# Optimization experiments

Hardware: AMD Instinct MI355X
Metric: run time of the kernel (lower is better)

## Reference

```python
import jax, jax.numpy as jnp
import numpy as np
from jax import lax

N, IN_CH, H, W = 8, 128, 160, 160
NUM_ANCHORS = 9
ANCHOR_SIZES = (32.0, 64.0, 128.0)
ANCHOR_RATIOS = (0.5, 1.0, 2.0)
NMS_THRESH = 0.7
PRE_NMS_TOPK = 6000
POST_NMS_TOPK = 1000
MIN_SIZE = 0.0
SCALE_CLAMP = float(np.log(1000.0 / 16.0))  # detectron2 Box2BoxTransform clamp


def setup_inputs():
    key = jax.random.key(0)
    k = jax.random.split(key, 4)
    std = 0.01  # nn.init.normal_(l.weight, std=0.01), bias = 0
    return {
        "feature_map": jax.random.normal(k[0], (N, IN_CH, H, W), jnp.float32),
        "conv1_w": jax.random.normal(k[1], (IN_CH, IN_CH, 3, 3), jnp.float32) * std,
        "conv1_b": jnp.zeros((IN_CH,), jnp.float32),
        "cls_w": jax.random.normal(k[2], (NUM_ANCHORS, IN_CH, 1, 1), jnp.float32) * std,
        "cls_b": jnp.zeros((NUM_ANCHORS,), jnp.float32),
        "box_w": jax.random.normal(k[3], (NUM_ANCHORS * 4, IN_CH, 1, 1), jnp.float32) * std,
        "box_b": jnp.zeros((NUM_ANCHORS * 4,), jnp.float32),
        "image_size": 1280,
    }


def _conv(x, w, b, pad):
    y = lax.conv_general_dilated(x, w, (1, 1), pad, dimension_numbers=("NCHW", "OIHW", "NCHW"))
    return y + b[None, :, None, None]


def _make_anchors(stride):
    # base anchors: area = size^2, w = sqrt(area/ratio), h = w*ratio (detectron2 style)
    base = []
    for s in ANCHOR_SIZES:
        area = s * s
        for r in ANCHOR_RATIOS:
            bw = np.sqrt(area / r)
            bh = bw * r
            base.append([-bw / 2.0, -bh / 2.0, bw / 2.0, bh / 2.0])
    base = jnp.asarray(np.array(base, np.float32))  # [A,4]
    sx = jnp.arange(W, dtype=jnp.float32) * stride
    sy = jnp.arange(H, dtype=jnp.float32) * stride
    yy, xx = jnp.meshgrid(sy, sx, indexing="ij")
    shifts = jnp.stack([xx, yy, xx, yy], axis=-1).reshape(-1, 1, 4)  # [H*W,1,4]
    return (shifts + base[None]).reshape(-1, 4)  # [H*W*A,4], (H,W,A) order


def _decode(deltas, anchors):
    # Box2BoxTransform.apply_deltas with weights (1,1,1,1)
    wa = anchors[:, 2] - anchors[:, 0]
    ha = anchors[:, 3] - anchors[:, 1]
    cxa = anchors[:, 0] + 0.5 * wa
    cya = anchors[:, 1] + 0.5 * ha
    dx, dy = deltas[..., 0], deltas[..., 1]
    dw = jnp.minimum(deltas[..., 2], SCALE_CLAMP)
    dh = jnp.minimum(deltas[..., 3], SCALE_CLAMP)
    cx = dx * wa + cxa
    cy = dy * ha + cya
    w = jnp.exp(dw) * wa
    h = jnp.exp(dh) * ha
    return jnp.stack([cx - 0.5 * w, cy - 0.5 * h, cx + 0.5 * w, cy + 0.5 * h], axis=-1)


def _nms_per_image(boxes, scores, image_size):
    # boxes [M,4], scores [M] -> top-PRE_NMS_TOPK, clip, filter, greedy NMS, keep POST_NMS_TOPK
    k = min(PRE_NMS_TOPK, scores.shape[0])
    top_scores, idx = lax.top_k(scores, k)
    b = jnp.clip(boxes[idx], 0.0, image_size)
    bw = b[:, 2] - b[:, 0]
    bh = b[:, 3] - b[:, 1]
    valid = (bw >= MIN_SIZE) & (bh >= MIN_SIZE)
    sc0 = jnp.where(valid, top_scores, -jnp.inf)
    areas = bw * bh

    def body(sc, _):
        i = jnp.argmax(sc)
        s = sc[i]
        bi = b[i]
        ix1 = jnp.maximum(bi[0], b[:, 0])
        iy1 = jnp.maximum(bi[1], b[:, 1])
        ix2 = jnp.minimum(bi[2], b[:, 2])
        iy2 = jnp.minimum(bi[3], b[:, 3])
        inter = jnp.maximum(ix2 - ix1, 0.0) * jnp.maximum(iy2 - iy1, 0.0)
        iou = inter / jnp.maximum(areas[i] + areas - inter, 1e-9)
        sc = jnp.where(iou > NMS_THRESH, -jnp.inf, sc)  # also suppresses self
        return sc, (i, s)

    _, (keep_idx, keep_sc) = lax.scan(body, sc0, None, length=POST_NMS_TOPK)
    ok = jnp.isfinite(keep_sc)
    out_boxes = jnp.where(ok[:, None], b[keep_idx], 0.0)
    out_scores = jnp.where(ok, keep_sc, jnp.float32(-1e9))
    return out_boxes, out_scores  # already sorted by descending objectness


def reference(feature_map, conv1_w, conv1_b, cls_w, cls_b, box_w, box_b, image_size):
    x = jax.nn.relu(_conv(feature_map, conv1_w, conv1_b, ((1, 1), (1, 1))))
    logits = _conv(x, cls_w, cls_b, ((0, 0), (0, 0)))  # [N,A,H,W]
    deltas = _conv(x, box_w, box_b, ((0, 0), (0, 0)))  # [N,4A,H,W]
    stride = float(round(image_size / W))
    anchors = _make_anchors(stride)  # [H*W*A,4]
    scores = logits.transpose(0, 2, 3, 1).reshape(N, -1)  # [N,HWA]
    d = deltas.reshape(N, NUM_ANCHORS, 4, H, W).transpose(0, 3, 4, 1, 2).reshape(N, -1, 4)
    proposals = _decode(d, anchors)  # [N,HWA,4]
    img = float(image_size)
    boxes, sc = jax.vmap(lambda bb, ss: _nms_per_image(bb, ss, img))(proposals, scores)
    return boxes, sc  # [N,POST_NMS_TOPK,4], [N,POST_NMS_TOPK]
```

## Files before the change

kernel.cpp:

```cpp
#include <hip/hip_runtime.h>
#include <stdint.h>
#include <math.h>

namespace {

constexpr int kH = 160, kW = 160, kN = 8;
constexpr int kHW = kH * kW;
constexpr int kM = kHW * 9;
constexpr int kPre = 6000;
constexpr int kPost = 1000;
constexpr int kCand = 6016;
constexpr int kScr = 7168;
constexpr int kWords = 94;
constexpr int kRowW = 96;
constexpr int kBmW = kM / 32;
constexpr double kClampD = 4.135166556742356;

typedef short short8 __attribute__((ext_vector_type(8)));
typedef float f32x4 __attribute__((ext_vector_type(4)));

__constant__ float c_hw[9] = {
  22.627416997969522f, 16.0f, 11.313708498984761f,
  45.254833995939045f, 32.0f, 22.627416997969522f,
  90.509667991878090f, 64.0f, 45.254833995939045f};
__constant__ float c_hh[9] = {
  11.313708498984761f, 16.0f, 22.627416997969522f,
  22.627416997969522f, 32.0f, 45.254833995939045f,
  45.254833995939045f, 64.0f, 90.509667991878090f};

__device__ __forceinline__ uint64_t ordd(double d) {
  uint64_t u = (uint64_t)__double_as_longlong(d);
  return (u >> 63) ? ~u : (u | 0x8000000000000000ull);
}
__device__ __forceinline__ unsigned ordf(float f) {
  unsigned u = __float_as_uint(f);
  return (u & 0x80000000u) ? ~u : (u | 0x80000000u);
}
__device__ __forceinline__ float4 ld4(const float* p) {
  return *reinterpret_cast<const float4*>(p);
}
__device__ __forceinline__ unsigned short f2bf(float f) {
  unsigned u = __float_as_uint(f);
  unsigned r = (u + 0x7FFFu + ((u >> 16) & 1u)) >> 16;
  return (unsigned short)r;
}
__device__ __forceinline__ uint64_t shfl64(uint64_t v, int src) {
  unsigned lo = __shfl((unsigned)v, src);
  unsigned hi = __shfl((unsigned)(v >> 32), src);
  return ((uint64_t)hi << 32) | lo;
}

__device__ __forceinline__ void hist_add(unsigned* hist, unsigned bucket, bool active) {
  uint64_t same = __ballot(active ? 1 : 0);
  #pragma unroll
  for (int b = 0; b < 8; ++b) {
    uint64_t bb = __ballot((bucket >> b) & 1u);
    same &= ((bucket >> b) & 1u) ? bb : ~bb;
  }
  if (active) {
    int lane = (int)(threadIdx.x & 63);
    int leader = __ffsll((unsigned long long)same) - 1;
    if (lane == leader) atomicAdd(&hist[bucket], (unsigned)__popcll((unsigned long long)same));
  }
}

__global__ __launch_bounds__(256) void prep_kernel(
    const float* __restrict__ w1, float* __restrict__ wT4,
    short* __restrict__ wBf)
{
  int i = blockIdx.x * 256 + (int)threadIdx.x;
  if (i < 1152 * 128) {
    int R = i >> 7, oc = i & 127;
    wT4[(size_t)(R >> 2) * 512 + oc * 4 + (R & 3)] = w1[(size_t)oc * 1152 + R];
    int ic = i & 127, q = i >> 7;
    int oc2 = q & 127, k9 = q >> 7;
    wBf[i] = (short)f2bf(w1[(size_t)oc2 * 1152 + ic * 9 + k9]);
  }
}

struct SConv {
  union {
    unsigned short A[3 * 162 * 32];
    unsigned short X[160 * 136];
  } u;
  float w9[9][128];
};

__global__ __launch_bounds__(256) void conv_mfma_kernel(
    const float* __restrict__ feat, const short* __restrict__ wBf,
    const float* __restrict__ b1f, const float* __restrict__ cw,
    const float* __restrict__ cb, unsigned* __restrict__ scoresU)
{
  __shared__ SConv sm;
  const int h = blockIdx.x, n = blockIdx.y;
  const int t = threadIdx.x;
  const int lane = t & 63, wave = t >> 6;
  const int l15 = lane & 15, l4 = lane >> 4;
  const float* fbase = feat + (size_t)n * 128 * kHW;

  f32x4 acc[10][2];
  #pragma unroll
  for (int mf = 0; mf < 10; ++mf)
    #pragma unroll
    for (int nf = 0; nf < 2; ++nf)
      #pragma unroll
      for (int r = 0; r < 4; ++r) acc[mf][nf][r] = 0.f;

  for (int i = t; i < 1152; i += 256) sm.w9[i >> 7][i & 127] = cw[i];

  for (int ib = 0; ib < 4; ++ib) {
    __syncthreads();
    #pragma unroll
    for (int pair = 0; pair < 3; ++pair) {
      int p = wave + 4 * pair;
      int R = p >> 2, icb = p & 3;
      int hh = h - 1 + R;
      bool rowok = (unsigned)hh < (unsigned)kH;
      for (int pxi = 0; pxi < 3; ++pxi) {
        int px = lane + 64 * pxi;
        if (px >= 162) break;
        int w = px - 1;
        bool ok = rowok && (unsigned)w < (unsigned)kW;
        const float* gp = fbase + ((size_t)(ib * 32 + icb * 8) * kH + hh) * kW + w;
        short8 v;
        #pragma unroll
        for (int j = 0; j < 8; ++j) {
          float f = ok ? gp[(size_t)j * kHW] : 0.f;
          v[j] = (short)f2bf(f);
        }
        int row = R * 162 + px;
        int chunk = icb ^ (row & 3) ^ ((row >> 2) & 3);
        *(short8*)&sm.u.A[(row * 4 + chunk) * 8] = v;
      }
    }
    __syncthreads();
    const int myoc0 = wave * 32;
    for (int k9 = 0; k9 < 9; ++k9) {
      int ky = k9 / 3, kx = k9 - 3 * ky;
      const short* wb = wBf + ((size_t)k9 * 128 + myoc0 + l15) * 128 + ib * 32 + 8 * l4;
      short8 bf0 = *(const short8*)wb;
      short8 bf1 = *(const short8*)(wb + 16 * 128);
      #pragma unroll
      for (int mf = 0; mf < 10; ++mf) {
        int row = ky * 162 + mf * 16 + l15 + kx;
        int chunk = l4 ^ (row & 3) ^ ((row >> 2) & 3);
        short8 af = *(const short8*)&sm.u.A[(row * 4 + chunk) * 8];
        acc[mf][0] = __builtin_amdgcn_mfma_f32_16x16x32_bf16(af, bf0, acc[mf][0], 0, 0, 0);
        acc[mf][1] = __builtin_amdgcn_mfma_f32_16x16x32_bf16(af, bf1, acc[mf][1], 0, 0, 0);
      }
    }
  }
  __syncthreads();
  float b1v[2] = { b1f[wave * 32 + l15], b1f[wave * 32 + 16 + l15] };
  #pragma unroll
  for (int mf = 0; mf < 10; ++mf)
    #pragma unroll
    for (int nf = 0; nf < 2; ++nf) {
      int oc = wave * 32 + nf * 16 + l15;
      #pragma unroll
      for (int reg = 0; reg < 4; ++reg) {
        int px = mf * 16 + l4 * 4 + reg;
        float v = fmaxf(acc[mf][nf][reg] + b1v[nf], 0.f);
        sm.u.X[px * 136 + oc] = f2bf(v);
      }
    }
  __syncthreads();
  for (int idx = t; idx < 1440; idx += 256) {
    int o = idx / 160, px = idx - 160 * o;
    const float* wr = sm.w9[o];
    float s = 0.f;
    #pragma unroll 4
    for (int c8 = 0; c8 < 16; ++c8) {
      short8 xv = *(const short8*)&sm.u.X[px * 136 + c8 * 8];
      #pragma unroll
      for (int j = 0; j < 8; ++j) {
        float xf = __uint_as_float(((unsigned)(unsigned short)xv[j]) << 16);
        s = fmaf(xf, wr[c8 * 8 + j], s);
      }
    }
    scoresU[(size_t)n * kM + ((size_t)h * kW + px) * 9 + o] = ordf(s + cb[o]);
  }
}

__global__ __launch_bounds__(1024) void screen_kernel(
    const unsigned* __restrict__ scoresU, unsigned* __restrict__ candIdx,
    unsigned* __restrict__ eqbuf)
{
  const int img = blockIdx.x;
  const unsigned* sc = scoresU + (size_t)img * kM;
  __shared__ unsigned hist[256];
  __shared__ unsigned bitmap[kBmW];
  __shared__ unsigned ssum[1024];
  __shared__ unsigned sh_prefix, sh_pmask, sh_K, sh_cg, sh_ce, sh_ip, sh_im, sh_Ki;
  const int t = threadIdx.x;
  if (t == 0) { sh_prefix = 0; sh_pmask = 0; sh_K = kScr; }
  for (int i = t; i < kBmW; i += 1024) bitmap[i] = 0;
  __syncthreads();
  for (int pass = 0; pass < 4; ++pass) {
    const int shift = 24 - pass * 8;
    if (t < 256) hist[t] = 0;
    __syncthreads();
    unsigned prefix = sh_prefix, pmask = sh_pmask;
    #pragma unroll 4
    for (int i = t; i < kM; i += 1024) {
      unsigned u = sc[i];
      bool active = ((u & pmask) == prefix);
      unsigned b = (u >> shift) & 255u;
      if (pass == 0) hist_add(hist, b, active);
      else if (active) atomicAdd(&hist[b], 1u);
    }
    __syncthreads();
    if (t == 0) {
      unsigned c = 0; int b = 255;
      for (; b > 0; --b) { unsigned hh = hist[b]; if (c + hh >= sh_K) break; c += hh; }
      sh_prefix |= ((unsigned)b) << shift;
      sh_pmask  |= 0xFFu << shift;
      sh_K -= c;
    }
    __syncthreads();
  }
  const unsigned T = sh_prefix;
  const unsigned need = sh_K;
  if (t == 0) { sh_cg = 0; sh_ce = 0; }
  __syncthreads();
  unsigned* eq = eqbuf + (size_t)img * 8192;
  #pragma unroll 4
  for (int i = t; i < kM; i += 1024) {
    unsigned u = sc[i];
    if (u > T) {
      atomicOr(&bitmap[(unsigned)i >> 5], 1u << (i & 31));
      atomicAdd(&sh_cg, 1u);
    } else if (u == T) {
      unsigned p = atomicAdd(&sh_ce, 1u);
      if (p < 8192u) eq[p] = (unsigned)i;
    }
  }
  __syncthreads();
  unsigned ce = sh_ce; if (ce > 8192u) ce = 8192u;
  if (ce == need) {
    for (unsigned j = t; j < need; j += 1024) {
      unsigned v = eq[j];
      atomicOr(&bitmap[v >> 5], 1u << (v & 31));
    }
  } else {
    if (t == 0) { sh_ip = 0; sh_im = 0; sh_Ki = need; }
    __syncthreads();
    for (int pass = 0; pass < 3; ++pass) {
      const int shift = 12 - pass * 6;
      if (t < 64) hist[t] = 0;
      __syncthreads();
      unsigned prefix = sh_ip, pmask = sh_im;
      for (unsigned i = t; i < ce; i += 1024) {
        unsigned v = eq[i];
        if ((v & pmask) == prefix) atomicAdd(&hist[(v >> shift) & 63u], 1u);
      }
      __syncthreads();
      if (t == 0) {
        unsigned c = 0; int b = 0;
        for (; b < 63; ++b) { unsigned hh = hist[b]; if (c + hh >= sh_Ki) break; c += hh; }
        sh_ip |= ((unsigned)b) << shift;
        sh_im |= 63u << shift;
        sh_Ki -= c;
      }
      __syncthreads();
    }
    const unsigned tau = sh_ip;
    for (unsigned i = t; i < ce; i += 1024) {
      unsigned v = eq[i];
      if (v <= tau) atomicOr(&bitmap[v >> 5], 1u << (v & 31));
    }
  }
  __syncthreads();
  unsigned cl = 0;
  #pragma unroll
  for (int k = 0; k < 8; ++k) {
    int wi = t * 8 + k;
    if (wi < kBmW) cl += (unsigned)__popc(bitmap[wi]);
  }
  ssum[t] = cl;
  __syncthreads();
  for (int o2 = 1; o2 < 1024; o2 <<= 1) {
    unsigned v = (t >= o2) ? ssum[t - o2] : 0u;
    __syncthreads();
    ssum[t] += v;
    __syncthreads();
  }
  unsigned off = ssum[t] - cl;
  unsigned* tout = candIdx + (size_t)img * kScr;
  #pragma unroll
  for (int k = 0; k < 8; ++k) {
    int wi = t * 8 + k;
    if (wi < kBmW) {
      unsigned wv = bitmap[wi];
      while (wv) {
        int b = __ffs(wv) - 1;
        wv &= wv - 1;
        tout[off++] = (unsigned)(wi * 32 + b);
      }
    }
  }
}

__global__ __launch_bounds__(256) void refine_kernel(
    const float* __restrict__ feat, const float* __restrict__ wT4,
    const float* __restrict__ b1, const float* __restrict__ cw,
    const float* __restrict__ cb, const float* __restrict__ bwp,
    const float* __restrict__ bbp, const unsigned* __restrict__ candIdx,
    double* __restrict__ rsc, double* __restrict__ rdd, int sBase)
{
  const int img = blockIdx.y;
  const int s0 = sBase + blockIdx.x * 6;
  const int t = threadIdx.x;
  __shared__ __align__(16) float patch[6][1160];
  __shared__ double xa[128][6];
  __shared__ double dd[6][5];
  __shared__ unsigned meta[6];
  if (t < 6) {
    int s = s0 + t;
    meta[t] = candIdx[(size_t)img * kScr + (s < kScr ? s : kScr - 1)];
  }
  __syncthreads();
  const float* fb = feat + (size_t)img * 128 * kHW;
  for (int e = t; e < 6 * 384; e += 256) {
    int rr = e / 384, q = e % 384, ic = q / 3, ky = q % 3;
    unsigned idx = meta[rr];
    int pix = (int)(idx / 9u);
    int hh = pix / kW - 1 + ky, ww = pix % kW;
    float v0 = 0.f, v1 = 0.f, v2 = 0.f;
    if ((unsigned)hh < (unsigned)kH) {
      const float* row = fb + ((size_t)ic * kH + hh) * kW + ww;
      if (ww - 1 >= 0) v0 = row[-1];
      v1 = row[0];
      if (ww + 1 < kW) v2 = row[1];
    }
    float* pp = &patch[rr][ic * 9 + ky * 3];
    pp[0] = v0; pp[1] = v1; pp[2] = v2;
  }
  __syncthreads();
  const int ocb = t & 31, rh = t >> 5;
  double acc[4][6];
  #pragma unroll
  for (int k = 0; k < 4; ++k)
    #pragma unroll
    for (int c = 0; c < 6; ++c) acc[k][c] = 0.0;
  {
    const float4* wq = reinterpret_cast<const float4*>(wT4) + (size_t)(rh * 36) * 128;
    for (int R4 = 0; R4 < 36; ++R4) {
      float4 wv0 = wq[(size_t)R4 * 128 + ocb];
      float4 wv1 = wq[(size_t)R4 * 128 + ocb + 32];
      float4 wv2 = wq[(size_t)R4 * 128 + ocb + 64];
      float4 wv3 = wq[(size_t)R4 * 128 + ocb + 96];
      double w0x = (double)wv0.x, w0y = (double)wv0.y, w0z = (double)wv0.z, w0w = (double)wv0.w;
      double w1x = (double)wv1.x, w1y = (double)wv1.y, w1z = (double)wv1.z, w1w = (double)wv1.w;
      double w2x = (double)wv2.x, w2y = (double)wv2.y, w2z = (double)wv2.z, w2w = (double)wv2.w;
      double w3x = (double)wv3.x, w3y = (double)wv3.y, w3z = (double)wv3.z, w3w = (double)wv3.w;
      const int Rp = rh * 144 + R4 * 4;
      #pragma unroll
      for (int c = 0; c < 6; ++c) {
        float4 pv = *reinterpret_cast<const float4*>(&patch[c][Rp]);
        double p0 = (double)pv.x, p1 = (double)pv.y,
               p2 = (double)pv.z, p3 = (double)pv.w;
        acc[0][c] = fma(w0x, p0, acc[0][c]);
        acc[0][c] = fma(w0y, p1, acc[0][c]);
        acc[0][c] = fma(w0z, p2, acc[0][c]);
        acc[0][c] = fma(w0w, p3, acc[0][c]);
        acc[1][c] = fma(w1x, p0, acc[1][c]);
        acc[1][c] = fma(w1y, p1, acc[1][c]);
        acc[1][c] = fma(w1z, p2, acc[1][c]);
        acc[1][c] = fma(w1w, p3, acc[1][c]);
        acc[2][c] = fma(w2x, p0, acc[2][c]);
        acc[2][c] = fma(w2y, p1, acc[2][c]);
        acc[2][c] = fma(w2z, p2, acc[2][c]);
        acc[2][c] = fma(w2w, p3, acc[2][c]);
        acc[3][c] = fma(w3x, p0, acc[3][c]);
        acc[3][c] = fma(w3y, p1, acc[3][c]);
        acc[3][c] = fma(w3z, p2, acc[3][c]);
        acc[3][c] = fma(w3w, p3, acc[3][c]);
      }
    }
  }
  #pragma unroll
  for (int g = 0; g < 8; ++g) {
    if (rh == g) {
      #pragma unroll
      for (int k = 0; k < 4; ++k)
        #pragma unroll
        for (int c = 0; c < 6; ++c) {
          if (g == 0) xa[ocb + 32 * k][c] = acc[k][c];
          else        xa[ocb + 32 * k][c] += acc[k][c];
        }
    }
    __syncthreads();
  }
  if (rh == 0) {
    #pragma unroll
    for (int k = 0; k < 4; ++k) {
      double bb1 = (double)b1[ocb + 32 * k];
      #pragma unroll
      for (int c = 0; c < 6; ++c)
        xa[ocb + 32 * k][c] = fmax(xa[ocb + 32 * k][c] + bb1, 0.0);
    }
  }
  __syncthreads();
  if (t < 30) {
    int rr = t % 6, j = t / 6;
    unsigned idx = meta[rr];
    int a = (int)(idx % 9u);
    const float* wr = (j < 4) ? (bwp + (size_t)(a * 4 + j) * 128)
                              : (cw + (size_t)a * 128);
    double s = 0.0;
    for (int c = 0; c < 128; ++c) s = fma((double)wr[c], xa[c][rr], s);
    dd[rr][j] = s + (double)((j < 4) ? bbp[a * 4 + j] : cb[a]);
  }
  __syncthreads();
  if (t < 6 && s0 + t < kScr) {
    size_t s = (size_t)img * kScr + s0 + t;
    rsc[s] = dd[t][4];
    double* rd = rdd + s * 4;
    rd[0] = dd[t][0]; rd[1] = dd[t][1]; rd[2] = dd[t][2]; rd[3] = dd[t][3];
  }
}

__global__ __launch_bounds__(1024) void select_sort_decode_kernel(
    const double* __restrict__ rsc, const double* __restrict__ rdd,
    const unsigned* __restrict__ candIdx, const int* __restrict__ imgsz,
    double* __restrict__ cand)
{
  const int img = blockIdx.x;
  const int t = threadIdx.x;
  __shared__ uint64_t k64[8192];
  __shared__ unsigned id32[8192];
  for (int j = t; j < 8192; j += 1024) {
    if (j < kScr) {
      k64[j] = ordd(rsc[(size_t)img * kScr + j]);
      id32[j] = (candIdx[(size_t)img * kScr + j] << 13) | (unsigned)j;
    } else { k64[j] = 0; id32[j] = 0xFFFFFFFFu; }
  }
  __syncthreads();
  for (unsigned kk = 2; kk <= 8192; kk <<= 1) {
    for (unsigned jj = kk >> 1; jj > 0; jj >>= 1) {
      for (unsigned i = t; i < 8192; i += 1024) {
        unsigned ixj = i ^ jj;
        if (ixj > i) {
          uint64_t ka = k64[i], kb = k64[ixj];
          unsigned ia = id32[i], ib = id32[ixj];
          bool desc = ((i & kk) == 0);
          bool amis = (ka < kb) || (ka == kb && ia > ib);
          if (desc ? amis : !amis) {
            k64[i] = kb; k64[ixj] = ka;
            id32[i] = ib; id32[ixj] = ia;
          }
        }
      }
      __syncthreads();
    }
  }
  double* cx1 = cand + (size_t)img * 6 * kCand;
  double* cy1 = cx1 + kCand; double* cx2 = cy1 + kCand; double* cy2 = cx2 + kCand;
  double* car = cy2 + kCand; double* csc = car + kCand;
  const double img_f = (double)imgsz[0];
  const double stride = floor(img_f / (double)kW + 0.5);
  for (int r = t; r < kCand; r += 1024) {
    if (r < kPre) {
      unsigned id = id32[r];
      unsigned slot = id & 8191u;
      unsigned aidx = id >> 13;
      int a = (int)(aidx % 9u);
      int pix = (int)(aidx / 9u);
      int hh = pix / kW, ww = pix % kW;
      double sx = (double)ww * stride, sy = (double)hh * stride;
      double hwd = (double)c_hw[a], hhd = (double)c_hh[a];
      double a0 = sx - hwd, a1 = sy - hhd, a2 = sx + hwd, a3 = sy + hhd;
      double wa = a2 - a0, ha = a3 - a1;
      double cxa = a0 + 0.5 * wa, cya = a1 + 0.5 * ha;
      const double* d = rdd + ((size_t)img * kScr + slot) * 4;
      double dx = d[0], dy = d[1];
      double dw = fmin(d[2], kClampD), dh = fmin(d[3], kClampD);
      double cx = dx * wa + cxa, cy = dy * ha + cya;
      double bw2 = exp(dw) * wa, bh2 = exp(dh) * ha;
      double x1 = cx - 0.5 * bw2, y1 = cy - 0.5 * bh2;
      double x2 = cx + 0.5 * bw2, y2 = cy + 0.5 * bh2;
      x1 = fmin(fmax(x1, 0.0), img_f); y1 = fmin(fmax(y1, 0.0), img_f);
      x2 = fmin(fmax(x2, 0.0), img_f); y2 = fmin(fmax(y2, 0.0), img_f);
      cx1[r] = x1; cy1[r] = y1; cx2[r] = x2; cy2[r] = y2;
      car[r] = (x2 - x1) * (y2 - y1);
      csc[r] = rsc[(size_t)img * kScr + slot];
    } else {
      cx1[r] = 0.0; cy1[r] = 0.0; cx2[r] = 0.0; cy2[r] = 0.0;
      car[r] = 0.0; csc[r] = -1e9;
    }
  }
}

__global__ __launch_bounds__(64) void mask_kernel(
    const double* __restrict__ cand, uint64_t* __restrict__ mask)
{
  const int img = blockIdx.z, bi = blockIdx.y, b8 = blockIdx.x;
  if (bi >= (b8 + 1) * 8) return;
  const int i = bi * 64 + (int)threadIdx.x;
  const double* cx1 = cand + (size_t)img * 6 * kCand;
  const double* cy1 = cx1 + kCand; const double* cx2 = cy1 + kCand;
  const double* cy2 = cx2 + kCand; const double* car = cy2 + kCand;
  __shared__ float jb[5][512];
  const int j0base = b8 * 512;
  for (int e = (int)threadIdx.x; e < 512; e += 64) {
    int j = j0base + e; if (j >= kCand) j = kCand - 1;
    jb[0][e] = (float)cx1[j]; jb[1][e] = (float)cy1[j];
    jb[2][e] = (float)cx2[j]; jb[3][e] = (float)cy2[j];
    jb[4][e] = (float)car[j];
  }
  const double x1d = cx1[i], y1d = cy1[i], x2d = cx2[i], y2d = cy2[i], ard = car[i];
  const float fx1 = (float)x1d, fy1 = (float)y1d, fx2 = (float)x2d,
              fy2 = (float)y2d, far2 = (float)ard;
  __syncthreads();
  uint64_t row[8];
  #pragma unroll
  for (int wi = 0; wi < 8; ++wi) {
    const int w = b8 * 8 + wi;
    uint64_t bits = 0;
    if (w < kWords) {
      const int e0 = wi * 64;
      uint64_t amb = 0;
      for (int jj = 0; jj < 64; ++jj) {
        const int e = e0 + jj;
        float ix1 = fmaxf(fx1, jb[0][e]);
        float iy1 = fmaxf(fy1, jb[1][e]);
        float ix2 = fminf(fx2, jb[2][e]);
        float iy2 = fminf(fy2, jb[3][e]);
        float inter = fmaxf(ix2 - ix1, 0.f) * fmaxf(iy2 - iy1, 0.f);
        float den = fmaxf(far2 + jb[4][e] - inter, 1e-9f);
        float lhs = fmaf(-0.7f, den, inter);
        bits |= (uint64_t)(lhs > 0.f) << jj;
        amb  |= (uint64_t)(fabsf(lhs) < 32.f) << jj;
      }
      while (amb) {
        int jj = __ffsll((unsigned long long)amb) - 1;
        amb &= amb - 1;
        int j = j0base + wi * 64 + jj;
        double ix1 = fmax(x1d, cx1[j]);
        double iy1 = fmax(y1d, cy1[j]);
        double ix2 = fmin(x2d, cx2[j]);
        double iy2 = fmin(y2d, cy2[j]);
        double inter = fmax(ix2 - ix1, 0.0) * fmax(iy2 - iy1, 0.0);
        double den = fmax(ard + car[j] - inter, 1e-9);
        uint64_t bit = (uint64_t)(inter > 0.7 * den);
        bits = (bits & ~(1ull << jj)) | (bit << jj);
      }
    }
    row[wi] = bits;
  }
  uint64_t* rp = mask + ((size_t)img * kCand + i) * kRowW + b8 * 8;
  #pragma unroll
  for (int wi = 0; wi < 8; ++wi)
    if (b8 * 8 + wi < kWords) rp[wi] = row[wi];
}

__global__ __launch_bounds__(256) void scan_kernel(
    const double* __restrict__ cand, const uint64_t* __restrict__ mask,
    float* __restrict__ out)
{
  const int img = blockIdx.x;
  const int t = threadIdx.x;
  const int lane = t & 63, wave = t >> 6;
  __shared__ uint64_t rows[2][64][96];
  __shared__ unsigned short keep[kPost];
  __shared__ int sh_cnt;
  if (t == 0) sh_cnt = 0;
  const uint64_t* mb = mask + (size_t)img * kCand * kRowW;
  const bool hiValid = (lane + 64 < kWords);
  uint64_t remLo = 0, remHi = 0;
  int cnt = 0;

  {
    uint64_t tl[16], th[16];
    #pragma unroll
    for (int i = 0; i < 16; ++i) {
      const uint64_t* rp = mb + (size_t)(wave + 4 * i) * kRowW;
      tl[i] = rp[lane];
      th[i] = hiValid ? rp[lane + 64] : 0ull;
    }
    #pragma unroll
    for (int i = 0; i < 16; ++i) {
      int r = wave + 4 * i;
      rows[0][r][lane] = tl[i];
      if (hiValid) rows[0][r][lane + 64] = th[i];
    }
  }
  __syncthreads();

  int cur = 0;
  for (int b = 0; b < kWords; ++b) {
    if (wave != 0) {
      int nb = b + 1;
      if (nb < kWords) {
        const uint64_t* rb = mb + (size_t)nb * 64 * kRowW;
        uint64_t tl[22], th[22];
        #pragma unroll
        for (int i = 0; i < 22; ++i) {
          int r = (wave - 1) + 3 * i;
          if (r < 64) {
            const uint64_t* rp = rb + (size_t)r * kRowW;
            tl[i] = rp[lane];
            th[i] = hiValid ? rp[lane + 64] : 0ull;
          }
        }
        #pragma unroll
        for (int i = 0; i < 22; ++i) {
          int r = (wave - 1) + 3 * i;
          if (r < 64) {
            rows[cur ^ 1][r][lane] = tl[i];
            if (hiValid) rows[cur ^ 1][r][lane + 64] = th[i];
          }
        }
      }
    } else {
      uint64_t rw = (b < 64) ? remLo : remHi;
      uint64_t aliveW = ~shfl64(rw, b & 63);
      if (b == kWords - 1) aliveW &= (1ull << 48) - 1ull;
      while (aliveW != 0ull && cnt < kPost) {
        int i = __ffsll((unsigned long long)aliveW) - 1;
        if (lane == 0) keep[cnt] = (unsigned short)(b * 64 + i);
        ++cnt;
        remLo |= rows[cur][i][lane];
        if (hiValid) remHi |= rows[cur][i][lane + 64];
        aliveW &= ~(1ull << i);
        aliveW &= ~rows[cur][i][b];
      }
      if (lane == 0) sh_cnt = cnt;
    }
    __syncthreads();
    if (sh_cnt >= kPost) break;
    cur ^= 1;
  }

  __syncthreads();
  const int fcnt = sh_cnt;
  const double* cx1 = cand + (size_t)img * 6 * kCand;
  const double* cy1 = cx1 + kCand; const double* cx2 = cy1 + kCand;
  const double* cy2 = cx2 + kCand; const double* car = cy2 + kCand;
  const double* csc = car + kCand;
  for (int r = t; r < kPost; r += 256) {
    float b0 = 0.f, b1v = 0.f, b2 = 0.f, b3 = 0.f, s = -1e9f;
    if (r < fcnt) {
      int i = keep[r];
      b0 = (float)cx1[i]; b1v = (float)cy1[i];
      b2 = (float)cx2[i]; b3 = (float)cy2[i]; s = (float)csc[i];
    }
    float* ob = out + ((size_t)img * kPost + r) * 4;
    ob[0] = b0; ob[1] = b1v; ob[2] = b2; ob[3] = b3;
    out[(size_t)kN * kPost * 4 + (size_t)img * kPost + r] = s;
  }
}

}

extern "C" void kernel_launch(void* const* d_in, const int* in_sizes, int n_in,
                              void* d_out, int out_size, void* d_ws, size_t ws_size,
                              hipStream_t stream) {
  const float* feat = (const float*)d_in[0];
  const float* w1   = (const float*)d_in[1];
  const float* b1   = (const float*)d_in[2];
  const float* cw   = (const float*)d_in[3];
  const float* cb   = (const float*)d_in[4];
  const float* bwp  = (const float*)d_in[5];
  const float* bbp  = (const float*)d_in[6];
  const int*   imgsz = (const int*)d_in[7];
  float* out = (float*)d_out;
  char* ws = (char*)d_ws;

  size_t off = 0;
  auto take = [&](size_t sz) { size_t o = off; off += (sz + 255) & ~(size_t)255; return o; };
  size_t oWT4    = take((size_t)1152 * 128 * 4);
  size_t oWBf    = take((size_t)9 * 128 * 128 * 2);
  size_t oScrU   = take((size_t)kN * kM * 4);
  size_t oCandI  = take((size_t)kN * kScr * 4);
  size_t oEq     = take((size_t)kN * 8192 * 4);
  size_t oRsc    = take((size_t)kN * kScr * 8);
  size_t oRdd    = take((size_t)kN * kScr * 4 * 8);
  size_t oCand   = take((size_t)kN * 6 * kCand * 8);
  size_t oMask   = take((size_t)kN * kCand * kRowW * 8);
  if (ws_size < off) return;

  float*    wT4     = (float*)(ws + oWT4);
  short*    wBf     = (short*)(ws + oWBf);
  unsigned* scoresU = (unsigned*)(ws + oScrU);
  unsigned* candI   = (unsigned*)(ws + oCandI);
  unsigned* eqb     = (unsigned*)(ws + oEq);
  double*   rsc     = (double*)(ws + oRsc);
  double*   rdd     = (double*)(ws + oRdd);
  double*   cand    = (double*)(ws + oCand);
  uint64_t* mask    = (uint64_t*)(ws + oMask);

  hipLaunchKernelGGL(prep_kernel, dim3(576), dim3(256), 0, stream, w1, wT4, wBf);
  hipLaunchKernelGGL(conv_mfma_kernel, dim3(kH, kN), dim3(256), 0, stream,
                     feat, wBf, b1, cw, cb, scoresU);
  hipLaunchKernelGGL(screen_kernel, dim3(kN), dim3(1024), 0, stream,
                     scoresU, candI, eqb);
  hipLaunchKernelGGL(refine_kernel, dim3(598, kN), dim3(256), 0, stream,
                     feat, wT4, b1, cw, cb, bwp, bbp, candI, rsc, rdd, 0);
  hipLaunchKernelGGL(refine_kernel, dim3(597, kN), dim3(256), 0, stream,
                     feat, wT4, b1, cw, cb, bwp, bbp, candI, rsc, rdd, 3588);
  hipLaunchKernelGGL(select_sort_decode_kernel, dim3(kN), dim3(1024), 0, stream,
                     rsc, rdd, candI, imgsz, cand);
  hipLaunchKernelGGL(mask_kernel, dim3(12, kWords, kN), dim3(64), 0, stream,
                     cand, mask);
  hipLaunchKernelGGL(scan_kernel, dim3(kN), dim3(256), 0, stream,
                     cand, mask, out);
}
```

Measured before the change: 1.580 ms.

## Restructure top-K radix select to scan full scores once, refine on candidate list

The screening kernel used to do four full passes over all 230k scores per image to find the exact top-K threshold byte by byte. It now does one full histogram pass on the top byte, compacts the elements in the boundary bucket into a list, and runs the remaining three radix passes and the index tie-break only over that list. A fallback keeps full-array passes when the boundary bucket overflows the list, which adds code size and, in that path, extra full scans.

```diff
diff --git a/kernel.cpp b/kernel.cpp
--- a/kernel.cpp
+++ b/kernel.cpp
@@ -191,86 +191,162 @@
   __shared__ unsigned hist[256];
   __shared__ unsigned bitmap[kBmW];
   __shared__ unsigned ssum[1024];
-  __shared__ unsigned sh_prefix, sh_pmask, sh_K, sh_cg, sh_ce, sh_ip, sh_im, sh_Ki;
+  __shared__ unsigned shv[8];
   const int t = threadIdx.x;
-  if (t == 0) { sh_prefix = 0; sh_pmask = 0; sh_K = kScr; }
   for (int i = t; i < kBmW; i += 1024) bitmap[i] = 0;
-  __syncthreads();
-  for (int pass = 0; pass < 4; ++pass) {
-    const int shift = 24 - pass * 8;
-    if (t < 256) hist[t] = 0;
-    __syncthreads();
-    unsigned prefix = sh_prefix, pmask = sh_pmask;
-    #pragma unroll 4
-    for (int i = t; i < kM; i += 1024) {
-      unsigned u = sc[i];
-      bool active = ((u & pmask) == prefix);
-      unsigned b = (u >> shift) & 255u;
-      if (pass == 0) hist_add(hist, b, active);
-      else if (active) atomicAdd(&hist[b], 1u);
-    }
-    __syncthreads();
-    if (t == 0) {
-      unsigned c = 0; int b = 255;
-      for (; b > 0; --b) { unsigned hh = hist[b]; if (c + hh >= sh_K) break; c += hh; }
-      sh_prefix |= ((unsigned)b) << shift;
-      sh_pmask  |= 0xFFu << shift;
-      sh_K -= c;
-    }
-    __syncthreads();
-  }
-  const unsigned T = sh_prefix;
-  const unsigned need = sh_K;
-  if (t == 0) { sh_cg = 0; sh_ce = 0; }
-  __syncthreads();
+  if (t < 256) hist[t] = 0;
+  if (t < 8) shv[t] = 0;
+  __syncthreads();
+  #pragma unroll 4
+  for (int i = t; i < kM; i += 1024) {
+    unsigned u = sc[i];
+    hist_add(hist, u >> 24, true);
+  }
+  __syncthreads();
+  if (t == 0) {
+    unsigned c = 0; int b = 255;
+    for (; b > 0; --b) { unsigned hh = hist[b]; if (c + hh >= (unsigned)kScr) break; c += hh; }
+    shv[0] = (unsigned)b;
+    shv[1] = (unsigned)kScr - c;
+    shv[2] = 0;
+  }
+  __syncthreads();
+  const unsigned b0 = shv[0];
+  const unsigned needB = shv[1];
   unsigned* eq = eqbuf + (size_t)img * 8192;
   #pragma unroll 4
   for (int i = t; i < kM; i += 1024) {
-    unsigned u = sc[i];
-    if (u > T) {
+    unsigned tb = sc[i] >> 24;
+    if (tb > b0) {
       atomicOr(&bitmap[(unsigned)i >> 5], 1u << (i & 31));
-      atomicAdd(&sh_cg, 1u);
-    } else if (u == T) {
-      unsigned p = atomicAdd(&sh_ce, 1u);
+    } else if (tb == b0) {
+      unsigned p = atomicAdd(&shv[2], 1u);
       if (p < 8192u) eq[p] = (unsigned)i;
     }
   }
   __syncthreads();
-  unsigned ce = sh_ce; if (ce > 8192u) ce = 8192u;
-  if (ce == need) {
-    for (unsigned j = t; j < need; j += 1024) {
-      unsigned v = eq[j];
-      atomicOr(&bitmap[v >> 5], 1u << (v & 31));
-    }
-  } else {
-    if (t == 0) { sh_ip = 0; sh_im = 0; sh_Ki = need; }
+  const unsigned ce = shv[2];
+  if (ce <= 8192u) {
+    if (t == 0) { shv[3] = 0; shv[4] = 0; shv[5] = needB; }
+    __syncthreads();
+    for (int pass = 0; pass < 3; ++pass) {
+      const int shift = 16 - pass * 8;
+      if (t < 256) hist[t] = 0;
+      __syncthreads();
+      unsigned pre = shv[3], pm = shv[4];
+      for (unsigned i = t; i < ce; i += 1024) {
+        unsigned ul = sc[eq[i]] & 0x00FFFFFFu;
+        if ((ul & pm) == pre) atomicAdd(&hist[(ul >> shift) & 255u], 1u);
+      }
+      __syncthreads();
+      if (t == 0) {
+        unsigned c = 0; int b = 255;
+        for (; b > 0; --b) { unsigned hh = hist[b]; if (c + hh >= shv[5]) break; c += hh; }
+        shv[3] |= ((unsigned)b) << shift;
+        shv[4] |= 0xFFu << shift;
+        shv[5] -= c;
+      }
+      __syncthreads();
+    }
+    const unsigned Tlow = shv[3];
+    const unsigned needT = shv[5];
+    for (unsigned i = t; i < ce; i += 1024) {
+      unsigned idx = eq[i];
+      if ((sc[idx] & 0x00FFFFFFu) > Tlow)
+        atomicOr(&bitmap[idx >> 5], 1u << (idx & 31));
+    }
+    if (t == 0) { shv[6] = 0; shv[7] = 0; shv[2] = needT; }
     __syncthreads();
     for (int pass = 0; pass < 3; ++pass) {
       const int shift = 12 - pass * 6;
       if (t < 64) hist[t] = 0;
       __syncthreads();
-      unsigned prefix = sh_ip, pmask = sh_im;
+      unsigned pre = shv[6], pm = shv[7];
       for (unsigned i = t; i < ce; i += 1024) {
-        unsigned v = eq[i];
-        if ((v & pmask) == prefix) atomicAdd(&hist[(v >> shift) & 63u], 1u);
+        unsigned idx = eq[i];
+        if ((sc[idx] & 0x00FFFFFFu) == Tlow && (idx & pm) == pre)
+          atomicAdd(&hist[(idx >> shift) & 63u], 1u);
       }
       __syncthreads();
       if (t == 0) {
         unsigned c = 0; int b = 0;
-        for (; b < 63; ++b) { unsigned hh = hist[b]; if (c + hh >= sh_Ki) break; c += hh; }
-        sh_ip |= ((unsigned)b) << shift;
-        sh_im |= 63u << shift;
-        sh_Ki -= c;
-      }
-      __syncthreads();
-    }
-    const unsigned tau = sh_ip;
+        for (; b < 63; ++b) { unsigned hh = hist[b]; if (c + hh >= shv[2]) break; c += hh; }
+        shv[6] |= ((unsigned)b) << shift;
+        shv[7] |= 63u << shift;
+        shv[2] -= c;
+      }
+      __syncthreads();
+    }
+    const unsigned tau = shv[6];
     for (unsigned i = t; i < ce; i += 1024) {
-      unsigned v = eq[i];
-      if (v <= tau) atomicOr(&bitmap[v >> 5], 1u << (v & 31));
-    }
-  }
-  __syncthreads();
+      unsigned idx = eq[i];
+      if ((sc[idx] & 0x00FFFFFFu) == Tlow && idx <= tau)
+        atomicOr(&bitmap[idx >> 5], 1u << (idx & 31));
+    }
+    __syncthreads();
+  } else {
+    if (t == 0) { shv[3] = 0; shv[4] = 0; shv[5] = needB; }
+    __syncthreads();
+    for (int pass = 0; pass < 3; ++pass) {
+      const int shift = 16 - pass * 8;
+      if (t < 256) hist[t] = 0;
+      __syncthreads();
+      unsigned pre = shv[3], pm = shv[4];
+      for (int i = t; i < kM; i += 1024) {
+        unsigned u = sc[i];
+        if ((u >> 24) == b0) {
+          unsigned ul = u & 0x00FFFFFFu;
+          if ((ul & pm) == pre) atomicAdd(&hist[(ul >> shift) & 255u], 1u);
+        }
+      }
+      __syncthreads();
+      if (t == 0) {
+        unsigned c = 0; int b = 255;
+        for (; b > 0; --b) { unsigned hh = hist[b]; if (c + hh >= shv[5]) break; c += hh; }
+        shv[3] |= ((unsigned)b) << shift;
+        shv[4] |= 0xFFu << shift;
+        shv[5] -= c;
+      }
+      __syncthreads();
+    }
+    const unsigned Tlow = shv[3];
+    const unsigned needT = shv[5];
+    for (int i = t; i < kM; i += 1024) {
+      unsigned u = sc[i];
+      if ((u >> 24) == b0 && (u & 0x00FFFFFFu) > Tlow)
+        atomicOr(&bitmap[(unsigned)i >> 5], 1u << (i & 31));
+    }
+    if (t == 0) { shv[6] = 0; shv[7] = 0; shv[2] = needT; }
+    __syncthreads();
+    for (int pass = 0; pass < 3; ++pass) {
+      const int shift = 12 - pass * 6;
+      if (t < 64) hist[t] = 0;
+      __syncthreads();
+      unsigned pre = shv[6], pm = shv[7];
+      for (int i = t; i < kM; i += 1024) {
+        unsigned u = sc[i];
+        if ((u >> 24) == b0 && (u & 0x00FFFFFFu) == Tlow &&
+            (((unsigned)i) & pm) == pre)
+          atomicAdd(&hist[(((unsigned)i) >> shift) & 63u], 1u);
+      }
+      __syncthreads();
+      if (t == 0) {
+        unsigned c = 0; int b = 0;
+        for (; b < 63; ++b) { unsigned hh = hist[b]; if (c + hh >= shv[2]) break; c += hh; }
+        shv[6] |= ((unsigned)b) << shift;
+        shv[7] |= 63u << shift;
+        shv[2] -= c;
+      }
+      __syncthreads();
+    }
+    const unsigned tau = shv[6];
+    for (int i = t; i < kM; i += 1024) {
+      unsigned u = sc[i];
+      if ((u >> 24) == b0 && (u & 0x00FFFFFFu) == Tlow && (unsigned)i <= tau)
+        atomicOr(&bitmap[(unsigned)i >> 5], 1u << (i & 31));
+    }
+    __syncthreads();
+  }
   unsigned cl = 0;
   #pragma unroll
   for (int k = 0; k < 8; ++k) {
```

Measured after the change: 1.742 ms. 1.1x slower.
